# Optimization experiments

Hardware: AMD Instinct MI355X
Metric: run time of the kernel (lower is better)

## Reference

```python
import jax, jax.numpy as jnp
import numpy as np
import math

IN_DIM = 256
DQK = IN_DIM // 8


def setup_inputs() -> dict:
    key = jax.random.key(0)
    k = jax.random.split(key, 7)
    B, C, W = 4, IN_DIM, 4096
    x_0 = jax.random.normal(k[0], (B, C, W), dtype=jnp.float32)
    x_1 = jax.random.normal(k[1], (B, C, W), dtype=jnp.float32)
    s = 1.0 / math.sqrt(C)
    # 1x1 Conv1d == dense projection over channel dim: weight [out, in], bias [out]
    wq = jax.random.normal(k[2], (DQK, C), dtype=jnp.float32) * s
    bq = jax.random.normal(k[3], (DQK,), dtype=jnp.float32) * s
    wk = jax.random.normal(k[4], (DQK, C), dtype=jnp.float32) * s
    bk = jax.random.normal(k[5], (DQK,), dtype=jnp.float32) * s
    # torch init is zeros; use small random so the attention path contributes
    gamma = jax.random.normal(k[6], (1,), dtype=jnp.float32) * 0.1
    return {"x_0": x_0, "x_1": x_1, "wq": wq, "bq": bq, "wk": wk, "bk": bk, "gamma": gamma}


def reference(x_0, x_1, wq, bq, wk, bk, gamma):
    B, C, W0 = x_0.shape
    scale = 1.0 / math.sqrt(C)
    # 1x1 conv projections: [B, dqk, W]
    q = jnp.einsum('dc,bcw->bdw', wq, x_0) + bq[None, :, None]   # [B, dqk, W0]
    k = jnp.einsum('dc,bcw->bdw', wk, x_1) + bk[None, :, None]   # [B, dqk, W1]
    # energy = key^T @ query, scaled: [B, W1, W0]
    energy = jnp.einsum('bdm,bdn->bmn', k, q) * scale
    attention = jax.nn.softmax(energy, axis=-1)                  # softmax over W0
    # out = attention @ x_0^T -> [B, W1, C] -> permute to [B, C, W1]
    out = jnp.einsum('bmn,bcn->bcm', attention, x_0)
    out = gamma[0] * out + x_1
    return out, attention
```

## Files before the change

kernel.cpp:

```cpp
#include <hip/hip_runtime.h>
#include <stdint.h>

#define B_    4
#define C_    256
#define W_    4096
#define DQK_  32
#define NT64_ 64
#define TSZ_  16384

typedef short bf16x8 __attribute__((ext_vector_type(8)));
typedef float f32x4  __attribute__((ext_vector_type(4)));

__device__ __forceinline__ float fexp2f(float x){
#if __has_builtin(__builtin_amdgcn_exp2f)
  return __builtin_amdgcn_exp2f(x);
#else
  return exp2f(x);
#endif
}
__device__ __forceinline__ float frcpf(float x){
#if __has_builtin(__builtin_amdgcn_rcpf)
  return __builtin_amdgcn_rcpf(x);
#else
  return 1.0f / x;
#endif
}
__device__ __forceinline__ uint32_t cvtpk(float a, float b){
  uint32_t r;
  asm("v_cvt_pk_bf16_f32 %0, %1, %2" : "=v"(r) : "v"(a), "v"(b));
  return r;
}
__device__ __forceinline__ unsigned short bf16c(float f){
  return (unsigned short)cvtpk(f, f);
}

__global__ __launch_bounds__(512) void sa_prep(
    const float* __restrict__ x0, const float* __restrict__ x1,
    const float* __restrict__ wq, const float* __restrict__ bq,
    const float* __restrict__ wk, const float* __restrict__ bk,
    unsigned short* __restrict__ qf, unsigned short* __restrict__ kT,
    unsigned short* __restrict__ x0f)
{
  const int b    = blockIdx.y;
  const int nt   = blockIdx.x;
  const int tid  = threadIdx.x;
  const int lane = tid & 63;
  const int cq   = __builtin_amdgcn_readfirstlane(tid >> 6);
  const int n    = nt * 64 + lane;
  const int lr   = lane & 15, lg = lane >> 4;
  const size_t bw = (size_t)b * ((size_t)C_ * W_) + n;

  __shared__ union {
    unsigned short xs[256 * 68];
    float red[8][64][33];
  } sm;

  float accq[DQK_], acck[DQK_];
  #pragma unroll
  for (int d = 0; d < DQK_; ++d){ accq[d] = 0.f; acck[d] = 0.f; }

  const int c0 = cq * 32;
  for (int i = 0; i < 32; ++i){
    const int c = c0 + i;
    const size_t off = bw + (size_t)c * W_;
    const float v0 = x0[off];
    const float v1 = x1[off];
    sm.xs[c * 68 + lane] = bf16c(v0);
    #pragma unroll
    for (int d = 0; d < DQK_; ++d){
      accq[d] = fmaf(wq[d * C_ + c], v0, accq[d]);
      acck[d] = fmaf(wk[d * C_ + c], v1, acck[d]);
    }
  }

  {
    unsigned short* xt = x0f + (size_t)(b * NT64_ + nt) * TSZ_;
    #pragma unroll
    for (int ct = 0; ct < 2; ++ct)
      #pragma unroll
      for (int ks = 0; ks < 2; ++ks){
        uint4 v = *(const uint4*)&sm.xs[(c0 + ct * 16 + lr) * 68 + ks * 32 + lg * 8];
        *(uint4*)(xt + ((size_t)((cq * 2 + ct) * 2 + ks) * 64 + lane) * 8) = v;
      }
  }
  __syncthreads();

  #pragma unroll
  for (int d = 0; d < DQK_; ++d) sm.red[cq][lane][d] = accq[d];
  __syncthreads();
  {
    const int nl = tid & 63, dg = tid >> 6;
    const int d0 = dg * 4;
    float s[4];
    #pragma unroll
    for (int j = 0; j < 4; ++j){
      float t = bq[d0 + j];
      #pragma unroll
      for (int g = 0; g < 8; ++g) t += sm.red[g][nl][d0 + j];
      s[j] = t;
    }
    uint2 pk; pk.x = cvtpk(s[0], s[1]); pk.y = cvtpk(s[2], s[3]);
    const int ng = nt * 64 + nl;
    const size_t addr = (((size_t)b * 256 + (ng >> 4)) * 64
                         + (ng & 15) + ((dg >> 1) << 4)) * 8 + (dg & 1) * 4;
    *(uint2*)(qf + addr) = pk;
  }
  __syncthreads();

  #pragma unroll
  for (int d = 0; d < DQK_; ++d) sm.red[cq][lane][d] = acck[d];
  __syncthreads();
  {
    const float SCL = 0.0625f * 1.44269504088896340736f;
    const int nl = tid & 63, dg = tid >> 6;
    const int d0 = dg * 4;
    float s[4];
    #pragma unroll
    for (int j = 0; j < 4; ++j){
      float t = bk[d0 + j];
      #pragma unroll
      for (int g = 0; g < 8; ++g) t += sm.red[g][nl][d0 + j];
      s[j] = t * SCL;
    }
    uint2 pk; pk.x = cvtpk(s[0], s[1]); pk.y = cvtpk(s[2], s[3]);
    *(uint2*)(kT + ((size_t)b * W_ + nt * 64 + nl) * DQK_ + d0) = pk;
  }
}

__global__ __launch_bounds__(512, 4) void sa_fused(
    const unsigned short* __restrict__ qf, const unsigned short* __restrict__ kT,
    const unsigned short* __restrict__ x0f, const float* __restrict__ x1,
    const float* __restrict__ gamma,
    float* __restrict__ out, float* __restrict__ att)
{
  const int lb = blockIdx.x;
  const int b    = (lb & 7) >> 1;
  const int mblk = ((lb >> 3) << 1) | (lb & 1);
  const int m0 = mblk * 32;
  const int tid = threadIdx.x;
  const int lane = tid & 63;
  const int wid = tid >> 6;
  const int lr = lane & 15, lg = lane >> 4;
  const int mt = wid & 1, nq = wid >> 1;

  __shared__ __align__(16) unsigned short Plds[2][32 * 64];
  __shared__ float ssum[8][16];

  const bf16x8 kf = *(const bf16x8*)(kT + ((size_t)b * W_ + m0 + mt * 16 + lr) * DQK_ + lg * 8);
  const unsigned short* qfw = qf + ((size_t)b * 256 * 64 + (size_t)nq * 64 + lane) * 8;
  const unsigned short* afw = x0f + (size_t)b * NT64_ * TSZ_ + wid * 2048 + lane * 8;

  float ps = 0.f;
  {
    const unsigned short* qp = qfw + 2048;
    bf16x8 qv = *(const bf16x8*)qfw;
    for (int s = 0; s < NT64_; ++s){
      bf16x8 qn = *(const bf16x8*)qp;
      qp = (s == NT64_ - 2) ? qfw : (qp + 2048);
      f32x4 e = __builtin_amdgcn_mfma_f32_16x16x32_bf16(qv, kf, (f32x4){0.f,0.f,0.f,0.f}, 0, 0, 0);
      ps += fexp2f(e[0]) + fexp2f(e[1]) + fexp2f(e[2]) + fexp2f(e[3]);
      qv = qn;
    }
  }
  ps += __shfl_xor(ps, 16);
  ps += __shfl_xor(ps, 32);
  if (lane < 16) ssum[wid][lane] = ps;
  __syncthreads();
  const float is = frcpf(ssum[mt][lr] + ssum[mt + 2][lr] + ssum[mt + 4][lr] + ssum[mt + 6][lr]);

  f32x4 acc[2][2];
  #pragma unroll
  for (int ct = 0; ct < 2; ++ct)
    #pragma unroll
    for (int m2 = 0; m2 < 2; ++m2) acc[ct][m2] = (f32x4){0.f,0.f,0.f,0.f};

  const int mlocP = mt * 16 + lr;
  const int pw_off = mlocP * 64
      + (((nq * 2 + (lg >> 1)) ^ (mlocP & 7)) << 3) + (lg & 1) * 4;
  int pfo[2][2];
  #pragma unroll
  for (int m2 = 0; m2 < 2; ++m2){
    const int prow = m2 * 16 + lr;
    #pragma unroll
    for (int ks = 0; ks < 2; ++ks)
      pfo[m2][ks] = prow * 64 + (((ks * 4 + lg) ^ (prow & 7)) << 3);
  }

  const unsigned short* qp = qfw + 2048;
  const unsigned short* afp = afw + TSZ_;
  float* attw = att + ((size_t)b * W_ + m0 + mt * 16 + lr) * W_ + nq * 16 + lg * 4;

  bf16x8 qv = *(const bf16x8*)qfw;
  bf16x8 af0 = *(const bf16x8*)(afw);
  bf16x8 af1 = *(const bf16x8*)(afw + 512);
  bf16x8 af2 = *(const bf16x8*)(afw + 1024);
  bf16x8 af3 = *(const bf16x8*)(afw + 1536);

  for (int s = 0; s < NT64_; ++s){
    const int cur = s & 1;

    f32x4 e = __builtin_amdgcn_mfma_f32_16x16x32_bf16(qv, kf, (f32x4){0.f,0.f,0.f,0.f}, 0, 0, 0);
    f32x4 p;
    #pragma unroll
    for (int r = 0; r < 4; ++r) p[r] = fexp2f(e[r]) * is;
    uint2 pv; pv.x = cvtpk(p[0], p[1]); pv.y = cvtpk(p[2], p[3]);
    *(uint2*)(&Plds[cur][0] + pw_off) = pv;

    asm volatile("s_waitcnt lgkmcnt(0)" ::: "memory");
    __builtin_amdgcn_sched_barrier(0);
    __builtin_amdgcn_s_barrier();

    qv = *(const bf16x8*)qp;
    qp = (s == NT64_ - 2) ? qfw : (qp + 2048);
    bf16x8 an0 = *(const bf16x8*)(afp);
    bf16x8 an1 = *(const bf16x8*)(afp + 512);
    bf16x8 an2 = *(const bf16x8*)(afp + 1024);
    bf16x8 an3 = *(const bf16x8*)(afp + 1536);
    afp = (s == NT64_ - 2) ? afw : (afp + TSZ_);
    __builtin_nontemporal_store(p, (f32x4*)attw);
    attw += 64;

    const unsigned short* Pb = &Plds[cur][0];
    bf16x8 pf[2][2];
    __builtin_amdgcn_s_setprio(1);
    #pragma unroll
    for (int m2 = 0; m2 < 2; ++m2)
      #pragma unroll
      for (int ks = 0; ks < 2; ++ks)
        pf[m2][ks] = *(const bf16x8*)(Pb + pfo[m2][ks]);
    acc[0][0] = __builtin_amdgcn_mfma_f32_16x16x32_bf16(af0, pf[0][0], acc[0][0], 0, 0, 0);
    acc[0][1] = __builtin_amdgcn_mfma_f32_16x16x32_bf16(af0, pf[1][0], acc[0][1], 0, 0, 0);
    acc[0][0] = __builtin_amdgcn_mfma_f32_16x16x32_bf16(af1, pf[0][1], acc[0][0], 0, 0, 0);
    acc[0][1] = __builtin_amdgcn_mfma_f32_16x16x32_bf16(af1, pf[1][1], acc[0][1], 0, 0, 0);
    acc[1][0] = __builtin_amdgcn_mfma_f32_16x16x32_bf16(af2, pf[0][0], acc[1][0], 0, 0, 0);
    acc[1][1] = __builtin_amdgcn_mfma_f32_16x16x32_bf16(af2, pf[1][0], acc[1][1], 0, 0, 0);
    acc[1][0] = __builtin_amdgcn_mfma_f32_16x16x32_bf16(af3, pf[0][1], acc[1][0], 0, 0, 0);
    acc[1][1] = __builtin_amdgcn_mfma_f32_16x16x32_bf16(af3, pf[1][1], acc[1][1], 0, 0, 0);
    __builtin_amdgcn_s_setprio(0);

    af0 = an0; af1 = an1; af2 = an2; af3 = an3;
  }

  const float g = gamma[0];
  const float* x1b = x1 + (size_t)b * C_ * W_;
  float* outb = out + (size_t)b * C_ * W_;
  #pragma unroll
  for (int ct = 0; ct < 2; ++ct)
    #pragma unroll
    for (int m2 = 0; m2 < 2; ++m2)
      #pragma unroll
      for (int r = 0; r < 4; ++r){
        const int c = wid * 32 + ct * 16 + lg * 4 + r;
        const size_t idx = (size_t)c * W_ + m0 + m2 * 16 + lr;
        const float xv = __builtin_nontemporal_load(&x1b[idx]);
        __builtin_nontemporal_store(fmaf(g, acc[ct][m2][r], xv), &outb[idx]);
      }
}

extern "C" void kernel_launch(void* const* d_in, const int* in_sizes, int n_in,
                              void* d_out, int out_size, void* d_ws, size_t ws_size,
                              hipStream_t stream)
{
  (void)in_sizes; (void)n_in; (void)out_size; (void)ws_size;
  const float* x0    = (const float*)d_in[0];
  const float* x1    = (const float*)d_in[1];
  const float* wq    = (const float*)d_in[2];
  const float* bq    = (const float*)d_in[3];
  const float* wk    = (const float*)d_in[4];
  const float* bk    = (const float*)d_in[5];
  const float* gamma = (const float*)d_in[6];

  unsigned short* qf  = (unsigned short*)d_ws;
  unsigned short* kT  = qf + (size_t)B_ * W_ * DQK_;
  unsigned short* x0f = kT + (size_t)B_ * W_ * DQK_;

  float* out = (float*)d_out;
  float* att = out + (size_t)B_ * C_ * W_;

  sa_prep <<<dim3(64, 4), 512, 0, stream>>>(x0, x1, wq, bq, wk, bk, qf, kT, x0f);
  sa_fused<<<512, 512, 0, stream>>>(qf, kT, x0f, x1, gamma, out, att);
}
```

Before: 128.4 us.

## Double query rows per block to halve x0 and Q reloads

Each block now handles 64 output rows instead of 32, so every wave computes two 16-row energy tiles and accumulates four M sub-tiles in the PV matmul. This halves the grid to 256 blocks and halves the total global reads of the bf16 x0 and Q streams, since each loaded fragment now feeds twice as many MFMAs. The cost is more registers and shared memory per block (launch bounds lowered to 2) and fewer blocks, which may leave some of the 256 CUs idle or reduce latency hiding.

```diff
diff --git a/kernel.cpp b/kernel.cpp
--- a/kernel.cpp
+++ b/kernel.cpp
@@ -127,7 +127,7 @@
   }
 }
 
-__global__ __launch_bounds__(512, 4) void sa_fused(
+__global__ __launch_bounds__(512, 2) void sa_fused(
     const unsigned short* __restrict__ qf, const unsigned short* __restrict__ kT,
     const unsigned short* __restrict__ x0f, const float* __restrict__ x1,
     const float* __restrict__ gamma,
@@ -136,50 +136,58 @@
   const int lb = blockIdx.x;
   const int b    = (lb & 7) >> 1;
   const int mblk = ((lb >> 3) << 1) | (lb & 1);
-  const int m0 = mblk * 32;
+  const int m0 = mblk * 64;
   const int tid = threadIdx.x;
   const int lane = tid & 63;
   const int wid = tid >> 6;
   const int lr = lane & 15, lg = lane >> 4;
-  const int mt = wid & 1, nq = wid >> 1;
-
-  __shared__ __align__(16) unsigned short Plds[2][32 * 64];
-  __shared__ float ssum[8][16];
-
-  const bf16x8 kf = *(const bf16x8*)(kT + ((size_t)b * W_ + m0 + mt * 16 + lr) * DQK_ + lg * 8);
+  const int nq = wid >> 1;
+  const int mh = wid & 1;
+
+  __shared__ __align__(16) unsigned short Plds[2][64 * 64];
+  __shared__ float ssum[4][64];
+
+  const int row0 = mh * 32 + lr, row1 = row0 + 16;
+  const bf16x8 kf0 = *(const bf16x8*)(kT + ((size_t)b * W_ + m0 + row0) * DQK_ + lg * 8);
+  const bf16x8 kf1 = *(const bf16x8*)(kT + ((size_t)b * W_ + m0 + row1) * DQK_ + lg * 8);
   const unsigned short* qfw = qf + ((size_t)b * 256 * 64 + (size_t)nq * 64 + lane) * 8;
   const unsigned short* afw = x0f + (size_t)b * NT64_ * TSZ_ + wid * 2048 + lane * 8;
 
-  float ps = 0.f;
+  float ps0 = 0.f, ps1 = 0.f;
   {
     const unsigned short* qp = qfw + 2048;
     bf16x8 qv = *(const bf16x8*)qfw;
     for (int s = 0; s < NT64_; ++s){
       bf16x8 qn = *(const bf16x8*)qp;
       qp = (s == NT64_ - 2) ? qfw : (qp + 2048);
-      f32x4 e = __builtin_amdgcn_mfma_f32_16x16x32_bf16(qv, kf, (f32x4){0.f,0.f,0.f,0.f}, 0, 0, 0);
-      ps += fexp2f(e[0]) + fexp2f(e[1]) + fexp2f(e[2]) + fexp2f(e[3]);
+      f32x4 e0 = __builtin_amdgcn_mfma_f32_16x16x32_bf16(qv, kf0, (f32x4){0.f,0.f,0.f,0.f}, 0, 0, 0);
+      f32x4 e1 = __builtin_amdgcn_mfma_f32_16x16x32_bf16(qv, kf1, (f32x4){0.f,0.f,0.f,0.f}, 0, 0, 0);
+      ps0 += (fexp2f(e0[0]) + fexp2f(e0[1])) + (fexp2f(e0[2]) + fexp2f(e0[3]));
+      ps1 += (fexp2f(e1[0]) + fexp2f(e1[1])) + (fexp2f(e1[2]) + fexp2f(e1[3]));
       qv = qn;
     }
   }
-  ps += __shfl_xor(ps, 16);
-  ps += __shfl_xor(ps, 32);
-  if (lane < 16) ssum[wid][lane] = ps;
-  __syncthreads();
-  const float is = frcpf(ssum[mt][lr] + ssum[mt + 2][lr] + ssum[mt + 4][lr] + ssum[mt + 6][lr]);
-
-  f32x4 acc[2][2];
+  ps0 += __shfl_xor(ps0, 16); ps0 += __shfl_xor(ps0, 32);
+  ps1 += __shfl_xor(ps1, 16); ps1 += __shfl_xor(ps1, 32);
+  if (lane < 16){
+    ssum[nq][mh * 32 + lane]      = ps0;
+    ssum[nq][mh * 32 + 16 + lane] = ps1;
+  }
+  __syncthreads();
+  const float is0 = frcpf(ssum[0][row0] + ssum[1][row0] + ssum[2][row0] + ssum[3][row0]);
+  const float is1 = frcpf(ssum[0][row1] + ssum[1][row1] + ssum[2][row1] + ssum[3][row1]);
+
+  f32x4 acc[2][4];
   #pragma unroll
   for (int ct = 0; ct < 2; ++ct)
     #pragma unroll
-    for (int m2 = 0; m2 < 2; ++m2) acc[ct][m2] = (f32x4){0.f,0.f,0.f,0.f};
-
-  const int mlocP = mt * 16 + lr;
-  const int pw_off = mlocP * 64
-      + (((nq * 2 + (lg >> 1)) ^ (mlocP & 7)) << 3) + (lg & 1) * 4;
-  int pfo[2][2];
-  #pragma unroll
-  for (int m2 = 0; m2 < 2; ++m2){
+    for (int m2 = 0; m2 < 4; ++m2) acc[ct][m2] = (f32x4){0.f,0.f,0.f,0.f};
+
+  const int pw0 = row0 * 64 + (((nq * 2 + (lg >> 1)) ^ (row0 & 7)) << 3) + (lg & 1) * 4;
+  const int pw1 = row1 * 64 + (((nq * 2 + (lg >> 1)) ^ (row1 & 7)) << 3) + (lg & 1) * 4;
+  int pfo[4][2];
+  #pragma unroll
+  for (int m2 = 0; m2 < 4; ++m2){
     const int prow = m2 * 16 + lr;
     #pragma unroll
     for (int ks = 0; ks < 2; ++ks)
@@ -188,7 +196,8 @@
 
   const unsigned short* qp = qfw + 2048;
   const unsigned short* afp = afw + TSZ_;
-  float* attw = att + ((size_t)b * W_ + m0 + mt * 16 + lr) * W_ + nq * 16 + lg * 4;
+  float* attw0 = att + ((size_t)b * W_ + m0 + row0) * W_ + nq * 16 + lg * 4;
+  float* attw1 = attw0 + (size_t)16 * W_;
 
   bf16x8 qv = *(const bf16x8*)qfw;
   bf16x8 af0 = *(const bf16x8*)(afw);
@@ -199,12 +208,18 @@
   for (int s = 0; s < NT64_; ++s){
     const int cur = s & 1;
 
-    f32x4 e = __builtin_amdgcn_mfma_f32_16x16x32_bf16(qv, kf, (f32x4){0.f,0.f,0.f,0.f}, 0, 0, 0);
-    f32x4 p;
-    #pragma unroll
-    for (int r = 0; r < 4; ++r) p[r] = fexp2f(e[r]) * is;
-    uint2 pv; pv.x = cvtpk(p[0], p[1]); pv.y = cvtpk(p[2], p[3]);
-    *(uint2*)(&Plds[cur][0] + pw_off) = pv;
+    f32x4 e0 = __builtin_amdgcn_mfma_f32_16x16x32_bf16(qv, kf0, (f32x4){0.f,0.f,0.f,0.f}, 0, 0, 0);
+    f32x4 e1 = __builtin_amdgcn_mfma_f32_16x16x32_bf16(qv, kf1, (f32x4){0.f,0.f,0.f,0.f}, 0, 0, 0);
+    f32x4 p0, p1;
+    #pragma unroll
+    for (int r = 0; r < 4; ++r){
+      p0[r] = fexp2f(e0[r]) * is0;
+      p1[r] = fexp2f(e1[r]) * is1;
+    }
+    uint2 pv0; pv0.x = cvtpk(p0[0], p0[1]); pv0.y = cvtpk(p0[2], p0[3]);
+    uint2 pv1; pv1.x = cvtpk(p1[0], p1[1]); pv1.y = cvtpk(p1[2], p1[3]);
+    *(uint2*)(&Plds[cur][0] + pw0) = pv0;
+    *(uint2*)(&Plds[cur][0] + pw1) = pv1;
 
     asm volatile("s_waitcnt lgkmcnt(0)" ::: "memory");
     __builtin_amdgcn_sched_barrier(0);
@@ -217,25 +232,25 @@
     bf16x8 an2 = *(const bf16x8*)(afp + 1024);
     bf16x8 an3 = *(const bf16x8*)(afp + 1536);
     afp = (s == NT64_ - 2) ? afw : (afp + TSZ_);
-    __builtin_nontemporal_store(p, (f32x4*)attw);
-    attw += 64;
+    __builtin_nontemporal_store(p0, (f32x4*)attw0);
+    __builtin_nontemporal_store(p1, (f32x4*)attw1);
+    attw0 += 64; attw1 += 64;
 
     const unsigned short* Pb = &Plds[cur][0];
-    bf16x8 pf[2][2];
+    bf16x8 pf[4][2];
     __builtin_amdgcn_s_setprio(1);
     #pragma unroll
-    for (int m2 = 0; m2 < 2; ++m2)
+    for (int m2 = 0; m2 < 4; ++m2)
       #pragma unroll
       for (int ks = 0; ks < 2; ++ks)
         pf[m2][ks] = *(const bf16x8*)(Pb + pfo[m2][ks]);
-    acc[0][0] = __builtin_amdgcn_mfma_f32_16x16x32_bf16(af0, pf[0][0], acc[0][0], 0, 0, 0);
-    acc[0][1] = __builtin_amdgcn_mfma_f32_16x16x32_bf16(af0, pf[1][0], acc[0][1], 0, 0, 0);
-    acc[0][0] = __builtin_amdgcn_mfma_f32_16x16x32_bf16(af1, pf[0][1], acc[0][0], 0, 0, 0);
-    acc[0][1] = __builtin_amdgcn_mfma_f32_16x16x32_bf16(af1, pf[1][1], acc[0][1], 0, 0, 0);
-    acc[1][0] = __builtin_amdgcn_mfma_f32_16x16x32_bf16(af2, pf[0][0], acc[1][0], 0, 0, 0);
-    acc[1][1] = __builtin_amdgcn_mfma_f32_16x16x32_bf16(af2, pf[1][0], acc[1][1], 0, 0, 0);
-    acc[1][0] = __builtin_amdgcn_mfma_f32_16x16x32_bf16(af3, pf[0][1], acc[1][0], 0, 0, 0);
-    acc[1][1] = __builtin_amdgcn_mfma_f32_16x16x32_bf16(af3, pf[1][1], acc[1][1], 0, 0, 0);
+    #pragma unroll
+    for (int m2 = 0; m2 < 4; ++m2){
+      acc[0][m2] = __builtin_amdgcn_mfma_f32_16x16x32_bf16(af0, pf[m2][0], acc[0][m2], 0, 0, 0);
+      acc[0][m2] = __builtin_amdgcn_mfma_f32_16x16x32_bf16(af1, pf[m2][1], acc[0][m2], 0, 0, 0);
+      acc[1][m2] = __builtin_amdgcn_mfma_f32_16x16x32_bf16(af2, pf[m2][0], acc[1][m2], 0, 0, 0);
+      acc[1][m2] = __builtin_amdgcn_mfma_f32_16x16x32_bf16(af3, pf[m2][1], acc[1][m2], 0, 0, 0);
+    }
     __builtin_amdgcn_s_setprio(0);
 
     af0 = an0; af1 = an1; af2 = an2; af3 = an3;
@@ -247,7 +262,7 @@
   #pragma unroll
   for (int ct = 0; ct < 2; ++ct)
     #pragma unroll
-    for (int m2 = 0; m2 < 2; ++m2)
+    for (int m2 = 0; m2 < 4; ++m2)
       #pragma unroll
       for (int r = 0; r < 4; ++r){
         const int c = wid * 32 + ct * 16 + lg * 4 + r;
@@ -278,5 +293,5 @@
   float* att = out + (size_t)B_ * C_ * W_;
 
   sa_prep <<<dim3(64, 4), 512, 0, stream>>>(x0, x1, wq, bq, wk, bk, qf, kT, x0f);
-  sa_fused<<<512, 512, 0, stream>>>(qf, kT, x0f, x1, gamma, out, att);
-}
+  sa_fused<<<256, 512, 0, stream>>>(qf, kT, x0f, x1, gamma, out, att);
+}
```

Result: no change. 126.3 us (median of 2 runs) (-1.6%).

## Shrink fused attention block to 16 query rows with 4 waves each

Applied to the files above, without the earlier changes.

Halves the query-row tile per block from 32 to 16 and uses 4 waves of 256 threads instead of 8, launching 1024 blocks. Each wave now covers all 16 rows and 64 output channels, so it issues 8 MFMAs per step, and the x0 operand loads move inside the loop instead of being prefetched one step ahead. The intent is more, smaller blocks for better occupancy and load balance. In exchange, each x0 tile is reused across only 16 rows, which doubles total x0 traffic, and the loss of the explicit prefetch may expose load latency.

```diff
diff --git a/kernel.cpp b/kernel.cpp
--- a/kernel.cpp
+++ b/kernel.cpp
@@ -127,7 +127,7 @@
   }
 }
 
-__global__ __launch_bounds__(512, 4) void sa_fused(
+__global__ __launch_bounds__(256, 4) void sa_fused(
     const unsigned short* __restrict__ qf, const unsigned short* __restrict__ kT,
     const unsigned short* __restrict__ x0f, const float* __restrict__ x1,
     const float* __restrict__ gamma,
@@ -136,19 +136,19 @@
   const int lb = blockIdx.x;
   const int b    = (lb & 7) >> 1;
   const int mblk = ((lb >> 3) << 1) | (lb & 1);
-  const int m0 = mblk * 32;
+  const int m0 = mblk * 16;
   const int tid = threadIdx.x;
   const int lane = tid & 63;
   const int wid = tid >> 6;
   const int lr = lane & 15, lg = lane >> 4;
-  const int mt = wid & 1, nq = wid >> 1;
-
-  __shared__ __align__(16) unsigned short Plds[2][32 * 64];
-  __shared__ float ssum[8][16];
-
-  const bf16x8 kf = *(const bf16x8*)(kT + ((size_t)b * W_ + m0 + mt * 16 + lr) * DQK_ + lg * 8);
+  const int nq = wid;
+
+  __shared__ __align__(16) unsigned short Plds[2][16 * 64];
+  __shared__ float ssum[4][16];
+
+  const bf16x8 kf = *(const bf16x8*)(kT + ((size_t)b * W_ + m0 + lr) * DQK_ + lg * 8);
   const unsigned short* qfw = qf + ((size_t)b * 256 * 64 + (size_t)nq * 64 + lane) * 8;
-  const unsigned short* afw = x0f + (size_t)b * NT64_ * TSZ_ + wid * 2048 + lane * 8;
+  const unsigned short* afw = x0f + (size_t)b * NT64_ * TSZ_ + wid * 4096 + lane * 8;
 
   float ps = 0.f;
   {
@@ -158,44 +158,29 @@
       bf16x8 qn = *(const bf16x8*)qp;
       qp = (s == NT64_ - 2) ? qfw : (qp + 2048);
       f32x4 e = __builtin_amdgcn_mfma_f32_16x16x32_bf16(qv, kf, (f32x4){0.f,0.f,0.f,0.f}, 0, 0, 0);
-      ps += fexp2f(e[0]) + fexp2f(e[1]) + fexp2f(e[2]) + fexp2f(e[3]);
+      ps += (fexp2f(e[0]) + fexp2f(e[1])) + (fexp2f(e[2]) + fexp2f(e[3]));
       qv = qn;
     }
   }
   ps += __shfl_xor(ps, 16);
   ps += __shfl_xor(ps, 32);
-  if (lane < 16) ssum[wid][lane] = ps;
-  __syncthreads();
-  const float is = frcpf(ssum[mt][lr] + ssum[mt + 2][lr] + ssum[mt + 4][lr] + ssum[mt + 6][lr]);
-
-  f32x4 acc[2][2];
-  #pragma unroll
-  for (int ct = 0; ct < 2; ++ct)
-    #pragma unroll
-    for (int m2 = 0; m2 < 2; ++m2) acc[ct][m2] = (f32x4){0.f,0.f,0.f,0.f};
-
-  const int mlocP = mt * 16 + lr;
-  const int pw_off = mlocP * 64
-      + (((nq * 2 + (lg >> 1)) ^ (mlocP & 7)) << 3) + (lg & 1) * 4;
-  int pfo[2][2];
-  #pragma unroll
-  for (int m2 = 0; m2 < 2; ++m2){
-    const int prow = m2 * 16 + lr;
-    #pragma unroll
-    for (int ks = 0; ks < 2; ++ks)
-      pfo[m2][ks] = prow * 64 + (((ks * 4 + lg) ^ (prow & 7)) << 3);
-  }
+  if (lane < 16) ssum[nq][lane] = ps;
+  __syncthreads();
+  const float is = frcpf(ssum[0][lr] + ssum[1][lr] + ssum[2][lr] + ssum[3][lr]);
+
+  f32x4 acc[4];
+  #pragma unroll
+  for (int ct = 0; ct < 4; ++ct) acc[ct] = (f32x4){0.f,0.f,0.f,0.f};
+
+  const int pw = lr * 64 + (((nq * 2 + (lg >> 1)) ^ (lr & 7)) << 3) + (lg & 1) * 4;
+  const int pfo0 = lr * 64 + (((0 * 4 + lg) ^ (lr & 7)) << 3);
+  const int pfo1 = lr * 64 + (((1 * 4 + lg) ^ (lr & 7)) << 3);
 
   const unsigned short* qp = qfw + 2048;
-  const unsigned short* afp = afw + TSZ_;
-  float* attw = att + ((size_t)b * W_ + m0 + mt * 16 + lr) * W_ + nq * 16 + lg * 4;
+  const unsigned short* afp = afw;
+  float* attw = att + ((size_t)b * W_ + m0 + lr) * W_ + nq * 16 + lg * 4;
 
   bf16x8 qv = *(const bf16x8*)qfw;
-  bf16x8 af0 = *(const bf16x8*)(afw);
-  bf16x8 af1 = *(const bf16x8*)(afw + 512);
-  bf16x8 af2 = *(const bf16x8*)(afw + 1024);
-  bf16x8 af3 = *(const bf16x8*)(afw + 1536);
-
   for (int s = 0; s < NT64_; ++s){
     const int cur = s & 1;
 
@@ -204,7 +189,7 @@
     #pragma unroll
     for (int r = 0; r < 4; ++r) p[r] = fexp2f(e[r]) * is;
     uint2 pv; pv.x = cvtpk(p[0], p[1]); pv.y = cvtpk(p[2], p[3]);
-    *(uint2*)(&Plds[cur][0] + pw_off) = pv;
+    *(uint2*)(&Plds[cur][0] + pw) = pv;
 
     asm volatile("s_waitcnt lgkmcnt(0)" ::: "memory");
     __builtin_amdgcn_sched_barrier(0);
@@ -212,49 +197,49 @@
 
     qv = *(const bf16x8*)qp;
     qp = (s == NT64_ - 2) ? qfw : (qp + 2048);
-    bf16x8 an0 = *(const bf16x8*)(afp);
-    bf16x8 an1 = *(const bf16x8*)(afp + 512);
-    bf16x8 an2 = *(const bf16x8*)(afp + 1024);
-    bf16x8 an3 = *(const bf16x8*)(afp + 1536);
-    afp = (s == NT64_ - 2) ? afw : (afp + TSZ_);
     __builtin_nontemporal_store(p, (f32x4*)attw);
     attw += 64;
 
     const unsigned short* Pb = &Plds[cur][0];
-    bf16x8 pf[2][2];
+    bf16x8 pf0 = *(const bf16x8*)(Pb + pfo0);
+    bf16x8 pf1 = *(const bf16x8*)(Pb + pfo1);
     __builtin_amdgcn_s_setprio(1);
-    #pragma unroll
-    for (int m2 = 0; m2 < 2; ++m2)
-      #pragma unroll
-      for (int ks = 0; ks < 2; ++ks)
-        pf[m2][ks] = *(const bf16x8*)(Pb + pfo[m2][ks]);
-    acc[0][0] = __builtin_amdgcn_mfma_f32_16x16x32_bf16(af0, pf[0][0], acc[0][0], 0, 0, 0);
-    acc[0][1] = __builtin_amdgcn_mfma_f32_16x16x32_bf16(af0, pf[1][0], acc[0][1], 0, 0, 0);
-    acc[0][0] = __builtin_amdgcn_mfma_f32_16x16x32_bf16(af1, pf[0][1], acc[0][0], 0, 0, 0);
-    acc[0][1] = __builtin_amdgcn_mfma_f32_16x16x32_bf16(af1, pf[1][1], acc[0][1], 0, 0, 0);
-    acc[1][0] = __builtin_amdgcn_mfma_f32_16x16x32_bf16(af2, pf[0][0], acc[1][0], 0, 0, 0);
-    acc[1][1] = __builtin_amdgcn_mfma_f32_16x16x32_bf16(af2, pf[1][0], acc[1][1], 0, 0, 0);
-    acc[1][0] = __builtin_amdgcn_mfma_f32_16x16x32_bf16(af3, pf[0][1], acc[1][0], 0, 0, 0);
-    acc[1][1] = __builtin_amdgcn_mfma_f32_16x16x32_bf16(af3, pf[1][1], acc[1][1], 0, 0, 0);
+    {
+      bf16x8 a0 = *(const bf16x8*)(afp);
+      bf16x8 a1 = *(const bf16x8*)(afp + 512);
+      bf16x8 a2 = *(const bf16x8*)(afp + 1024);
+      bf16x8 a3 = *(const bf16x8*)(afp + 1536);
+      acc[0] = __builtin_amdgcn_mfma_f32_16x16x32_bf16(a0, pf0, acc[0], 0, 0, 0);
+      acc[0] = __builtin_amdgcn_mfma_f32_16x16x32_bf16(a1, pf1, acc[0], 0, 0, 0);
+      acc[1] = __builtin_amdgcn_mfma_f32_16x16x32_bf16(a2, pf0, acc[1], 0, 0, 0);
+      acc[1] = __builtin_amdgcn_mfma_f32_16x16x32_bf16(a3, pf1, acc[1], 0, 0, 0);
+    }
+    {
+      bf16x8 a4 = *(const bf16x8*)(afp + 2048);
+      bf16x8 a5 = *(const bf16x8*)(afp + 2560);
+      bf16x8 a6 = *(const bf16x8*)(afp + 3072);
+      bf16x8 a7 = *(const bf16x8*)(afp + 3584);
+      acc[2] = __builtin_amdgcn_mfma_f32_16x16x32_bf16(a4, pf0, acc[2], 0, 0, 0);
+      acc[2] = __builtin_amdgcn_mfma_f32_16x16x32_bf16(a5, pf1, acc[2], 0, 0, 0);
+      acc[3] = __builtin_amdgcn_mfma_f32_16x16x32_bf16(a6, pf0, acc[3], 0, 0, 0);
+      acc[3] = __builtin_amdgcn_mfma_f32_16x16x32_bf16(a7, pf1, acc[3], 0, 0, 0);
+    }
     __builtin_amdgcn_s_setprio(0);
-
-    af0 = an0; af1 = an1; af2 = an2; af3 = an3;
+    afp += TSZ_;
   }
 
   const float g = gamma[0];
   const float* x1b = x1 + (size_t)b * C_ * W_;
   float* outb = out + (size_t)b * C_ * W_;
   #pragma unroll
-  for (int ct = 0; ct < 2; ++ct)
-    #pragma unroll
-    for (int m2 = 0; m2 < 2; ++m2)
-      #pragma unroll
-      for (int r = 0; r < 4; ++r){
-        const int c = wid * 32 + ct * 16 + lg * 4 + r;
-        const size_t idx = (size_t)c * W_ + m0 + m2 * 16 + lr;
-        const float xv = __builtin_nontemporal_load(&x1b[idx]);
-        __builtin_nontemporal_store(fmaf(g, acc[ct][m2][r], xv), &outb[idx]);
-      }
+  for (int ct = 0; ct < 4; ++ct)
+    #pragma unroll
+    for (int r = 0; r < 4; ++r){
+      const int c = wid * 64 + ct * 16 + lg * 4 + r;
+      const size_t idx = (size_t)c * W_ + m0 + lr;
+      const float xv = __builtin_nontemporal_load(&x1b[idx]);
+      __builtin_nontemporal_store(fmaf(g, acc[ct][r], xv), &outb[idx]);
+    }
 }
 
 extern "C" void kernel_launch(void* const* d_in, const int* in_sizes, int n_in,
@@ -278,5 +263,5 @@
   float* att = out + (size_t)B_ * C_ * W_;
 
   sa_prep <<<dim3(64, 4), 512, 0, stream>>>(x0, x1, wq, bq, wk, bk, qf, kT, x0f);
-  sa_fused<<<512, 512, 0, stream>>>(qf, kT, x0f, x1, gamma, out, att);
-}
+  sa_fused<<<1024, 256, 0, stream>>>(qf, kT, x0f, x1, gamma, out, att);
+}
```

New measurement: 220.0 us. +71.4%, slower.
